# Optimization experiments

Hardware: AMD Instinct MI355X
Metric: run time of the kernel (lower is better)

Reference implementation:

```python
import jax, jax.numpy as jnp
import numpy as np

TOPK = 13
NUM_CLASSES = 80
ALPHA = 1.0
BETA = 6.0
EPS = 1e-09
BS, NA, M = 8, 33600, 64
IMG = 1280.0


def setup_inputs() -> dict:
    key = jax.random.key(0)
    k = jax.random.split(key, 8)
    pd_scores = jax.random.uniform(k[0], (BS, NA, NUM_CLASSES), jnp.float32)
    pd_xy = jax.random.uniform(k[1], (BS, NA, 2), jnp.float32) * IMG
    pd_r = jax.random.uniform(k[2], (BS, NA, 1), jnp.float32) * 63.0 + 1.0
    pd_circles = jnp.concatenate([pd_xy, pd_r], axis=-1)
    anc_points = jax.random.uniform(k[3], (NA, 2), jnp.float32) * IMG
    gt_labels = jax.random.randint(k[4], (BS, M, 1), 0, NUM_CLASSES)
    gt_xy = jax.random.uniform(k[5], (BS, M, 2), jnp.float32) * IMG
    gt_r = jax.random.uniform(k[6], (BS, M, 1), jnp.float32) * 120.0 + 8.0
    gt_circles = jnp.concatenate([gt_xy, gt_r], axis=-1)
    mask_gt = (jax.random.uniform(k[7], (BS, M, 1)) > 0.2).astype(jnp.float32)
    return {"pd_scores": pd_scores, "pd_circles": pd_circles, "anc_points": anc_points,
            "gt_labels": gt_labels, "gt_circles": gt_circles, "mask_gt": mask_gt}


def _circle_iou(gt_circles, pd_circles):
    # gt_circles: (bs, M, 3); pd_circles: (bs, NA, 3) -> iou (bs, M, NA)
    c0 = gt_circles[:, :, None, :2]          # (bs, M, 1, 2)
    r0 = gt_circles[:, :, None, 2]           # (bs, M, 1)
    c1 = pd_circles[:, None, :, :2]          # (bs, 1, NA, 2)
    r1 = pd_circles[:, None, :, 2]           # (bs, 1, NA)
    d = jnp.sqrt(jnp.sum((c0 - c1) ** 2, axis=-1) + 1e-12)  # (bs, M, NA)
    # lens (partial-overlap) area, numerically safe
    d1 = (r0 ** 2 - r1 ** 2 + d ** 2) / (2.0 * d)
    d2 = d - d1
    a0 = r0 ** 2 * jnp.arccos(jnp.clip(d1 / jnp.maximum(r0, EPS), -1.0, 1.0)) \
         - d1 * jnp.sqrt(jnp.clip(r0 ** 2 - d1 ** 2, 0.0, None))
    a1 = r1 ** 2 * jnp.arccos(jnp.clip(d2 / jnp.maximum(r1, EPS), -1.0, 1.0)) \
         - d2 * jnp.sqrt(jnp.clip(r1 ** 2 - d2 ** 2, 0.0, None))
    lens = a0 + a1
    contained = jnp.pi * jnp.minimum(r0, r1) ** 2
    inter = jnp.where(d >= r0 + r1, 0.0, jnp.where(d <= jnp.abs(r0 - r1), contained, lens))
    area0 = jnp.pi * r0 ** 2
    area1 = jnp.pi * r1 ** 2
    union = area0 + area1 - inter
    return jnp.where(union > 0, inter / union, 0.0)


def _assigner(pd_scores, pd_circles, anc_points, gt_labels, gt_circles, mask_gt):
    bs, na, nc = pd_scores.shape
    m = gt_circles.shape[1]
    mask_gt_f = mask_gt[..., 0]  # (bs, m)

    # select_candidates_in_gts: anchor point inside gt circle
    d_anc = jnp.sqrt(jnp.sum((anc_points[None, None, :, :] - gt_circles[:, :, None, :2]) ** 2, axis=-1))
    mask_in_gts = (d_anc < gt_circles[:, :, None, 2]).astype(pd_scores.dtype)  # (bs, m, na)
    mask_valid = mask_in_gts * mask_gt_f[:, :, None]

    # get_box_metrics: gather class scores at gt label, circle IoU, align metric
    gl = jnp.clip(gt_labels[..., 0], 0, nc - 1)  # (bs, m) int
    ps_t = jnp.transpose(pd_scores, (0, 2, 1))   # (bs, nc, na)
    bbox_scores = jnp.take_along_axis(ps_t, jnp.broadcast_to(gl[:, :, None], (bs, m, na)), axis=1)
    bbox_scores = bbox_scores * mask_valid
    overlaps = _circle_iou(gt_circles, pd_circles) * mask_valid  # (bs, m, na)
    align_metric = (bbox_scores ** ALPHA) * (overlaps ** BETA)

    # select_topk_candidates
    topk_metrics, topk_idxs = jax.lax.top_k(align_metric, TOPK)   # (bs, m, topk)
    topk_mask = jnp.broadcast_to(mask_gt_f[:, :, None] > 0, topk_idxs.shape)
    topk_idxs = jnp.where(topk_mask, topk_idxs, 0)
    counts = jnp.zeros((bs, m, na), pd_scores.dtype).at[
        jnp.arange(bs)[:, None, None], jnp.arange(m)[None, :, None], topk_idxs].add(1.0)
    mask_topk = jnp.where(counts > 1, 0.0, counts)
    mask_pos = mask_topk * mask_in_gts * mask_gt_f[:, :, None]

    # select_highest_overlaps: resolve anchors assigned to multiple gts
    fg = jnp.sum(mask_pos, axis=1)                       # (bs, na)
    multi = (fg[:, None, :] > 1)                          # (bs, 1->m, na)
    max_idx = jnp.argmax(overlaps, axis=1)                # (bs, na)
    is_max = jax.nn.one_hot(max_idx, m, axis=1, dtype=mask_pos.dtype)  # (bs, m, na)
    mask_pos = jnp.where(multi, is_max, mask_pos)
    fg_mask = jnp.sum(mask_pos, axis=1)                   # (bs, na)
    target_gt_idx = jnp.argmax(mask_pos, axis=1)          # (bs, na)

    # get_targets
    bidx = jnp.arange(bs)[:, None]
    target_labels = jnp.clip(gt_labels[..., 0][bidx, target_gt_idx], 0, None)   # (bs, na)
    target_circles = gt_circles[bidx, target_gt_idx]                             # (bs, na, 3)
    target_scores = jax.nn.one_hot(target_labels, nc, dtype=pd_scores.dtype)
    target_scores = jnp.where(fg_mask[..., None] > 0, target_scores, 0.0)

    # normalize scores by aligned metric
    am = align_metric * mask_pos
    pos_align = jnp.max(am, axis=-1, keepdims=True)                # (bs, m, 1)
    pos_overlaps = jnp.max(overlaps * mask_pos, axis=-1, keepdims=True)
    norm = jnp.max(am * pos_overlaps / (pos_align + EPS), axis=1)[..., None]  # (bs, na, 1)
    target_scores = target_scores * norm
    return target_labels, target_circles, target_scores, fg_mask > 0, target_gt_idx


def reference(pd_scores, pd_circles, anc_points, gt_labels, gt_circles, mask_gt):
    return _assigner(pd_scores, pd_circles, anc_points, gt_labels, gt_circles, mask_gt)
```

## Files before the change

### kernel.cpp

```cpp
#include <hip/hip_runtime.h>
#include <math.h>

#define B   8
#define NA  33600
#define M   64
#define NC  80
#define KK  13
#define EPSF 1e-9f
#define PIF 3.14159265358979323846f

#define NPOS 1536
#define NBM  (B * M)
#define SPB  (M * KK)


__device__ __forceinline__ float circle_iou(float gx, float gy, float gr,
                                            float px, float py, float pr) {
    float dx = gx - px, dy = gy - py;
    float d  = sqrtf(dx * dx + dy * dy + 1e-12f);
    float r0sq = gr * gr, r1sq = pr * pr;
    float d1 = (r0sq - r1sq + d * d) / (2.0f * d);
    float d2 = d - d1;
    float t0 = fminf(fmaxf(d1 / fmaxf(gr, EPSF), -1.0f), 1.0f);
    float t1 = fminf(fmaxf(d2 / fmaxf(pr, EPSF), -1.0f), 1.0f);
    float a0 = r0sq * acosf(t0) - d1 * sqrtf(fmaxf(r0sq - d1 * d1, 0.0f));
    float a1 = r1sq * acosf(t1) - d2 * sqrtf(fmaxf(r1sq - d2 * d2, 0.0f));
    float lens = a0 + a1;
    float rmin = fminf(gr, pr);
    float contained = PIF * rmin * rmin;
    float inter = (d >= gr + pr) ? 0.0f
                : ((d <= fabsf(gr - pr)) ? contained : lens);
    float uni = PIF * r0sq + PIF * r1sq - inter;
    return (uni > 0.0f) ? inter / uni : 0.0f;
}


__global__ __launch_bounds__(1024)
void k_discover(const float* __restrict__ pd_scores, const float* __restrict__ pd_circles,
                const float* __restrict__ anc, const int* __restrict__ gt_labels,
                const float* __restrict__ gt_circles, const float* __restrict__ mask_gt,
                int* __restrict__ wlist, int* __restrict__ assigned,
                float* __restrict__ am_val) {
    int bid = blockIdx.x;
    int b   = bid & 7;
    int m   = bid >> 3;
    int bm  = b * M + m;
    int tid = threadIdx.x;

    const int SL = (B * NA) / NBM;
    int s0 = bid * SL;
    if (tid < SL) { assigned[s0 + tid] = -1; am_val[s0 + tid] = 0.0f; }

    __shared__ int   s_ccnt, s_pcnt;
    __shared__ int   s_ca[NPOS];
    __shared__ int   s_pa[NPOS];
    __shared__ float s_pv[NPOS];
    __shared__ int   s_win[KK];

    float gmask = mask_gt[bm];
    if (!(gmask > 0.0f)) {
        if (tid < KK) wlist[bm * KK + tid] = -1;
        return;
    }

    float gx = gt_circles[bm * 3 + 0];
    float gy = gt_circles[bm * 3 + 1];
    float gr = gt_circles[bm * 3 + 2];
    int gl = gt_labels[bm];
    gl = gl < 0 ? 0 : (gl > NC - 1 ? NC - 1 : gl);

    if (tid == 0) { s_ccnt = 0; s_pcnt = 0; }
    __syncthreads();

    for (int q = tid; q < NA / 2; q += 1024) {
        float4 ap = reinterpret_cast<const float4*>(anc)[q];
        float dx0 = ap.x - gx, dy0 = ap.y - gy;
        float dx1 = ap.z - gx, dy1 = ap.w - gy;
        bool h0 = sqrtf(dx0 * dx0 + dy0 * dy0) < gr;
        bool h1 = sqrtf(dx1 * dx1 + dy1 * dy1) < gr;
        if (h0) { int p = atomicAdd(&s_ccnt, 1); if (p < NPOS) s_ca[p] = 2 * q; }
        if (h1) { int p = atomicAdd(&s_ccnt, 1); if (p < NPOS) s_ca[p] = 2 * q + 1; }
    }
    __syncthreads();
    int ccnt = s_ccnt; if (ccnt > NPOS) ccnt = NPOS;

    for (int i = tid; i < ccnt; i += 1024) {
        int a = s_ca[i];
        size_t pb = ((size_t)b * NA + a) * 3;
        float px = pd_circles[pb + 0];
        float py = pd_circles[pb + 1];
        float pr = pd_circles[pb + 2];
        float cdx = gx - px, cdy = gy - py;
        float dc = sqrtf(cdx * cdx + cdy * cdy + 1e-12f);
        if (dc >= gr + pr) continue;
        float ov = circle_iou(gx, gy, gr, px, py, pr);
        if (!(ov > 0.0f)) continue;
        float sc = pd_scores[((size_t)b * NA + a) * NC + gl];
        float o2 = ov * ov;
        float met = sc * (o2 * o2 * o2);
        if (met > 0.0f) {
            int p = atomicAdd(&s_pcnt, 1);
            s_pa[p] = a; s_pv[p] = met;
        }
    }
    __syncthreads();
    int pcnt = s_pcnt;

    if (tid >= 64) return;

    for (int k = 0; k < KK; k++) {
        float bv = 0.0f; int ba = 0x7fffffff; int bp = -1;
        for (int i = tid; i < pcnt; i += 64) {
            float v = s_pv[i];
            if (v > 0.0f) {
                int a = s_pa[i];
                if (v > bv || (v == bv && a < ba)) { bv = v; ba = a; bp = i; }
            }
        }
        for (int off = 32; off > 0; off >>= 1) {
            float v2 = __shfl_xor(bv, off);
            int   a2 = __shfl_xor(ba, off);
            int   p2 = __shfl_xor(bp, off);
            if (v2 > bv || (v2 == bv && a2 < ba)) { bv = v2; ba = a2; bp = p2; }
        }
        if (tid == 0) {
            if (bp >= 0) { s_win[k] = ba; s_pv[bp] = -1.0f; }
            else s_win[k] = -2;
        }
    }

    int defmask = 0;
    for (int k = 0; k < KK; k++) if (s_win[k] == -2) defmask |= (1 << k);
    if (defmask) {
        int base = 0;
        while (defmask && base < NA) {
            int idx = base + tid;
            bool freez = (idx < NA);
            for (int i = 0; i < pcnt; i++)
                freez = freez && (s_pa[i] != idx);
            unsigned long long msk = __ballot(freez);
            while (msk && defmask) {
                int bit = __ffsll((long long)msk) - 1; msk &= msk - 1;
                int k2  = __ffs(defmask) - 1;          defmask &= defmask - 1;
                if (tid == 0) s_win[k2] = base + bit;
            }
            base += 64;
        }
        while (defmask) {
            int k2 = __ffs(defmask) - 1; defmask &= defmask - 1;
            if (tid == 0) s_win[k2] = -1;
        }
    }

    if (tid < KK) {
        int a = s_win[tid];
        int outv = -1;
        if (a >= 0) {
            float ax = anc[2 * a], ay = anc[2 * a + 1];
            float dx = ax - gx, dy = ay - gy;
            if (sqrtf(dx * dx + dy * dy) < gr) outv = a;
        }
        wlist[bm * KK + tid] = outv;
    }
}


__global__ __launch_bounds__(1024)
void k_resolve(const float* __restrict__ pd_scores, const float* __restrict__ pd_circles,
               const float* __restrict__ anc, const int* __restrict__ gt_labels,
               const float* __restrict__ gt_circles, const float* __restrict__ mask_gt,
               const int* __restrict__ wlist,
               int* __restrict__ assigned, float* __restrict__ am_val,
               int* __restrict__ pos_align_i, int* __restrict__ pos_ov_i) {
    int b = blockIdx.x;
    int tid = threadIdx.x;

    __shared__ unsigned int s_cnt[NA / 4 + 1];
    __shared__ float s_gx[M], s_gy[M], s_gr[M];
    __shared__ int   s_gl[M], s_act[M];
    __shared__ int   s_posa[M], s_poso[M];
    __shared__ int   s_multi[512];
    __shared__ int   s_nm;

    if (tid < M) {
        int gi = b * M + tid;
        s_act[tid] = mask_gt[gi] > 0.0f;
        s_gx[tid] = gt_circles[gi * 3 + 0];
        s_gy[tid] = gt_circles[gi * 3 + 1];
        s_gr[tid] = gt_circles[gi * 3 + 2];
        int l = gt_labels[gi];
        s_gl[tid] = l < 0 ? 0 : (l > NC - 1 ? NC - 1 : l);
        s_posa[tid] = 0; s_poso[tid] = 0;
    }
    if (tid == 0) s_nm = 0;
    for (int w = tid; w < NA / 4 + 1; w += 1024) s_cnt[w] = 0;
    __syncthreads();

    int a = -1, m = -1; unsigned int prev = 0;
    if (tid < SPB) {
        a = wlist[b * SPB + tid];
        m = tid / KK;
        if (a >= 0) {
            unsigned int sh = 8u * (a & 3);
            unsigned int old = atomicAdd(&s_cnt[a >> 2], 1u << sh);
            prev = (old >> sh) & 0xFFu;
        }
    }
    __syncthreads();

    bool single = false;
    if (a >= 0) {
        unsigned int c = (s_cnt[a >> 2] >> (8u * (a & 3))) & 0xFFu;
        if (c == 1u) single = true;
        else if (prev == 0u) { int i2 = atomicAdd(&s_nm, 1); s_multi[i2] = a; }
    }
    if (single) {
        int i = b * NA + a;
        float gx = s_gx[m], gy = s_gy[m], gr = s_gr[m];
        float px = pd_circles[(size_t)i * 3 + 0];
        float py = pd_circles[(size_t)i * 3 + 1];
        float pr = pd_circles[(size_t)i * 3 + 2];
        float cdx = gx - px, cdy = gy - py;
        float dc = sqrtf(cdx * cdx + cdy * cdy + 1e-12f);
        float ov = (dc >= gr + pr) ? 0.0f : circle_iou(gx, gy, gr, px, py, pr);
        float met = 0.0f;
        if (ov > 0.0f) {
            float sc = pd_scores[(size_t)i * NC + s_gl[m]];
            float o2 = ov * ov;
            met = sc * (o2 * o2 * o2);
        }
        assigned[i] = m;
        am_val[i]   = met;
        atomicMax(&s_posa[m], __float_as_int(met));
        atomicMax(&s_poso[m], __float_as_int(ov));
    }
    __syncthreads();

    int lane = tid & 63, w = tid >> 6;
    int nm = s_nm;
    for (int r = w; r < nm; r += 16) {
        int am_ = s_multi[r];
        int i = b * NA + am_;
        float ax = anc[2 * am_], ay = anc[2 * am_ + 1];
        float px = pd_circles[(size_t)i * 3 + 0];
        float py = pd_circles[(size_t)i * 3 + 1];
        float pr = pd_circles[(size_t)i * 3 + 2];
        float ov = 0.0f;
        if (s_act[lane]) {
            float gx = s_gx[lane], gy = s_gy[lane], gr = s_gr[lane];
            float dx = ax - gx, dy = ay - gy;
            if (sqrtf(dx * dx + dy * dy) < gr) {
                float cdx = gx - px, cdy = gy - py;
                float dc = sqrtf(cdx * cdx + cdy * cdy + 1e-12f);
                ov = (dc >= gr + pr) ? 0.0f : circle_iou(gx, gy, gr, px, py, pr);
            }
        }
        float bv = ov; int bmx = lane;
        for (int off = 32; off > 0; off >>= 1) {
            float v2 = __shfl_xor(bv, off);
            int   m2 = __shfl_xor(bmx, off);
            if (v2 > bv || (v2 == bv && m2 < bmx)) { bv = v2; bmx = m2; }
        }
        if (lane == 0) {
            float met = 0.0f;
            if (bv > 0.0f) {
                float sc = pd_scores[(size_t)i * NC + s_gl[bmx]];
                float o2 = bv * bv;
                met = sc * (o2 * o2 * o2);
            }
            assigned[i] = bmx;
            am_val[i]   = met;
            atomicMax(&s_posa[bmx], __float_as_int(met));
            atomicMax(&s_poso[bmx], __float_as_int(bv));
        }
    }
    __syncthreads();

    if (tid < M) {
        pos_align_i[b * M + tid] = s_posa[tid];
        pos_ov_i[b * M + tid]    = s_poso[tid];
    }
}


__global__ void k_out(const int* __restrict__ assigned, const float* __restrict__ am_val,
                      const int* __restrict__ pos_align_i, const int* __restrict__ pos_ov_i,
                      const int* __restrict__ gt_labels, const float* __restrict__ gt_circles,
                      float* __restrict__ out_labels, float* __restrict__ out_circ,
                      float* __restrict__ out_scores, float* __restrict__ out_fg,
                      float* __restrict__ out_gtidx) {
    const int QPR = NC / 4;
    int q = blockIdx.x * blockDim.x + threadIdx.x;
    if (q >= B * NA * QPR) return;
    int row = q / QPR;
    int c0  = (q - row * QPR) * 4;
    int b   = row / NA;

    int g = assigned[row];
    int gidx = 0; float fg = 0.0f; float norm = 0.0f;
    if (g >= 0) {
        gidx = g; fg = 1.0f;
        float pa = __int_as_float(pos_align_i[b * M + g]);
        float po = __int_as_float(pos_ov_i[b * M + g]);
        norm = am_val[row] * po / (pa + EPSF);
    }
    int rawl = gt_labels[b * M + gidx];
    int lbl = rawl < 0 ? 0 : rawl;

    float4 v = make_float4(0.f, 0.f, 0.f, 0.f);
    if (g >= 0) {
        int off = lbl - c0;
        if (off >= 0 && off < 4) ((float*)&v)[off] = norm;
    }
    reinterpret_cast<float4*>(out_scores)[q] = v;

    if (c0 == 0) {
        out_labels[row] = (float)lbl;
        out_circ[(size_t)row * 3 + 0] = gt_circles[(b * M + gidx) * 3 + 0];
        out_circ[(size_t)row * 3 + 1] = gt_circles[(b * M + gidx) * 3 + 1];
        out_circ[(size_t)row * 3 + 2] = gt_circles[(b * M + gidx) * 3 + 2];
        out_fg[row]    = fg;
        out_gtidx[row] = (float)gidx;
    }
}


extern "C" void kernel_launch(void* const* d_in, const int* in_sizes, int n_in,
                              void* d_out, int out_size, void* d_ws, size_t ws_size,
                              hipStream_t stream) {
    const float* pd_scores  = (const float*)d_in[0];
    const float* pd_circles = (const float*)d_in[1];
    const float* anc        = (const float*)d_in[2];
    const int*   gt_labels  = (const int*)  d_in[3];
    const float* gt_circles = (const float*)d_in[4];
    const float* mask_gt    = (const float*)d_in[5];

    char* w = (char*)d_ws;
    int*   wlist       = (int*)w;   w += (size_t)NBM * KK * sizeof(int);
    int*   assigned    = (int*)w;   w += (size_t)B * NA * sizeof(int);
    float* am_val      = (float*)w; w += (size_t)B * NA * sizeof(float);
    int*   pos_align_i = (int*)w;   w += (size_t)B * M * sizeof(int);
    int*   pos_ov_i    = (int*)w;   w += (size_t)B * M * sizeof(int);

    float* out        = (float*)d_out;
    float* out_labels = out;
    float* out_circ   = out_labels + (size_t)B * NA;
    float* out_scores = out_circ + (size_t)B * NA * 3;
    float* out_fg     = out_scores + (size_t)B * NA * NC;
    float* out_gtidx  = out_fg + (size_t)B * NA;

    k_discover<<<NBM, 1024, 0, stream>>>(pd_scores, pd_circles, anc, gt_labels,
                                         gt_circles, mask_gt,
                                         wlist, assigned, am_val);

    k_resolve<<<B, 1024, 0, stream>>>(pd_scores, pd_circles, anc, gt_labels,
                                      gt_circles, mask_gt, wlist,
                                      assigned, am_val, pos_align_i, pos_ov_i);

    int nq = B * NA * (NC / 4);
    k_out<<<(nq + 255) / 256, 256, 0, stream>>>(assigned, am_val,
                                                pos_align_i, pos_ov_i,
                                                gt_labels, gt_circles,
                                                out_labels, out_circ, out_scores,
                                                out_fg, out_gtidx);
}
```

Baseline: 73.78 us.

## Split resolve kernel per (batch, gt) block with global atomic maxima

The resolve stage moves from one 1024-thread block per batch to one 256-thread block per (batch, gt) pair. Each block finds duplicate anchors by scanning the 832-entry winner list instead of a per-batch shared-memory counter array. The per-gt max reductions now go through global atomicMax, and the discover kernel zero-initializes those arrays first. The goal is more parallelism in a tiny serial stage, at the cost of redundant list loads and scans per block plus global atomics.

```diff
diff --git a/kernel.cpp b/kernel.cpp
--- a/kernel.cpp
+++ b/kernel.cpp
@@ -40,7 +40,8 @@
                 const float* __restrict__ anc, const int* __restrict__ gt_labels,
                 const float* __restrict__ gt_circles, const float* __restrict__ mask_gt,
                 int* __restrict__ wlist, int* __restrict__ assigned,
-                float* __restrict__ am_val) {
+                float* __restrict__ am_val,
+                int* __restrict__ pos_align_i, int* __restrict__ pos_ov_i) {
     int bid = blockIdx.x;
     int b   = bid & 7;
     int m   = bid >> 3;
@@ -50,6 +51,7 @@
     const int SL = (B * NA) / NBM;
     int s0 = bid * SL;
     if (tid < SL) { assigned[s0 + tid] = -1; am_val[s0 + tid] = 0.0f; }
+    if (m == 0 && tid < M) { pos_align_i[b * M + tid] = 0; pos_ov_i[b * M + tid] = 0; }
 
     __shared__ int   s_ccnt, s_pcnt;
     __shared__ int   s_ca[NPOS];
@@ -165,21 +167,23 @@
 }
 
 
-__global__ __launch_bounds__(1024)
+__global__ __launch_bounds__(256)
 void k_resolve(const float* __restrict__ pd_scores, const float* __restrict__ pd_circles,
                const float* __restrict__ anc, const int* __restrict__ gt_labels,
                const float* __restrict__ gt_circles, const float* __restrict__ mask_gt,
                const int* __restrict__ wlist,
                int* __restrict__ assigned, float* __restrict__ am_val,
                int* __restrict__ pos_align_i, int* __restrict__ pos_ov_i) {
-    int b = blockIdx.x;
+    int bid = blockIdx.x;
+    int b   = bid & 7;
+    int m   = bid >> 3;
     int tid = threadIdx.x;
-
-    __shared__ unsigned int s_cnt[NA / 4 + 1];
+    int lane = tid & 63, w = tid >> 6;
+
+    __shared__ int   s_wl[SPB];
     __shared__ float s_gx[M], s_gy[M], s_gr[M];
     __shared__ int   s_gl[M], s_act[M];
-    __shared__ int   s_posa[M], s_poso[M];
-    __shared__ int   s_multi[512];
+    __shared__ int   s_multi[KK];
     __shared__ int   s_nm;
 
     if (tid < M) {
@@ -190,55 +194,48 @@
         s_gr[tid] = gt_circles[gi * 3 + 2];
         int l = gt_labels[gi];
         s_gl[tid] = l < 0 ? 0 : (l > NC - 1 ? NC - 1 : l);
-        s_posa[tid] = 0; s_poso[tid] = 0;
     }
     if (tid == 0) s_nm = 0;
-    for (int w = tid; w < NA / 4 + 1; w += 1024) s_cnt[w] = 0;
-    __syncthreads();
-
-    int a = -1, m = -1; unsigned int prev = 0;
-    if (tid < SPB) {
-        a = wlist[b * SPB + tid];
-        m = tid / KK;
-        if (a >= 0) {
-            unsigned int sh = 8u * (a & 3);
-            unsigned int old = atomicAdd(&s_cnt[a >> 2], 1u << sh);
-            prev = (old >> sh) & 0xFFu;
-        }
-    }
-    __syncthreads();
-
-    bool single = false;
-    if (a >= 0) {
-        unsigned int c = (s_cnt[a >> 2] >> (8u * (a & 3))) & 0xFFu;
-        if (c == 1u) single = true;
-        else if (prev == 0u) { int i2 = atomicAdd(&s_nm, 1); s_multi[i2] = a; }
-    }
-    if (single) {
-        int i = b * NA + a;
-        float gx = s_gx[m], gy = s_gy[m], gr = s_gr[m];
-        float px = pd_circles[(size_t)i * 3 + 0];
-        float py = pd_circles[(size_t)i * 3 + 1];
-        float pr = pd_circles[(size_t)i * 3 + 2];
-        float cdx = gx - px, cdy = gy - py;
-        float dc = sqrtf(cdx * cdx + cdy * cdy + 1e-12f);
-        float ov = (dc >= gr + pr) ? 0.0f : circle_iou(gx, gy, gr, px, py, pr);
-        float met = 0.0f;
-        if (ov > 0.0f) {
-            float sc = pd_scores[(size_t)i * NC + s_gl[m]];
-            float o2 = ov * ov;
-            met = sc * (o2 * o2 * o2);
-        }
-        assigned[i] = m;
-        am_val[i]   = met;
-        atomicMax(&s_posa[m], __float_as_int(met));
-        atomicMax(&s_poso[m], __float_as_int(ov));
-    }
-    __syncthreads();
-
-    int lane = tid & 63, w = tid >> 6;
+    for (int i = tid; i < SPB; i += 256) s_wl[i] = wlist[b * SPB + i];
+    __syncthreads();
+
+    if (w == 0) {
+        int myslot = m * KK + lane;
+        int mya = (lane < KK) ? s_wl[myslot] : -1;
+        int cnt = 0, minslot = SPB;
+        for (int i = 0; i < SPB; i++) {
+            int v = s_wl[i];
+            if (mya >= 0 && v == mya) { cnt++; if (i < minslot) minslot = i; }
+        }
+        if (mya >= 0 && minslot == myslot) {
+            if (cnt == 1) {
+                int i = b * NA + mya;
+                float gx = s_gx[m], gy = s_gy[m], gr = s_gr[m];
+                float px = pd_circles[(size_t)i * 3 + 0];
+                float py = pd_circles[(size_t)i * 3 + 1];
+                float pr = pd_circles[(size_t)i * 3 + 2];
+                float cdx = gx - px, cdy = gy - py;
+                float dc = sqrtf(cdx * cdx + cdy * cdy + 1e-12f);
+                float ov = (dc >= gr + pr) ? 0.0f : circle_iou(gx, gy, gr, px, py, pr);
+                float met = 0.0f;
+                if (ov > 0.0f) {
+                    float sc = pd_scores[(size_t)i * NC + s_gl[m]];
+                    float o2 = ov * ov;
+                    met = sc * (o2 * o2 * o2);
+                }
+                assigned[i] = m;
+                am_val[i]   = met;
+                atomicMax(&pos_align_i[b * M + m], __float_as_int(met));
+                atomicMax(&pos_ov_i[b * M + m],    __float_as_int(ov));
+            } else {
+                int p = atomicAdd(&s_nm, 1); s_multi[p] = mya;
+            }
+        }
+    }
+    __syncthreads();
+
     int nm = s_nm;
-    for (int r = w; r < nm; r += 16) {
+    for (int r = w; r < nm; r += 4) {
         int am_ = s_multi[r];
         int i = b * NA + am_;
         float ax = anc[2 * am_], ay = anc[2 * am_ + 1];
@@ -270,15 +267,9 @@
             }
             assigned[i] = bmx;
             am_val[i]   = met;
-            atomicMax(&s_posa[bmx], __float_as_int(met));
-            atomicMax(&s_poso[bmx], __float_as_int(bv));
-        }
-    }
-    __syncthreads();
-
-    if (tid < M) {
-        pos_align_i[b * M + tid] = s_posa[tid];
-        pos_ov_i[b * M + tid]    = s_poso[tid];
+            atomicMax(&pos_align_i[b * M + bmx], __float_as_int(met));
+            atomicMax(&pos_ov_i[b * M + bmx],    __float_as_int(bv));
+        }
     }
 }
 
@@ -351,11 +342,12 @@
 
     k_discover<<<NBM, 1024, 0, stream>>>(pd_scores, pd_circles, anc, gt_labels,
                                          gt_circles, mask_gt,
-                                         wlist, assigned, am_val);
-
-    k_resolve<<<B, 1024, 0, stream>>>(pd_scores, pd_circles, anc, gt_labels,
-                                      gt_circles, mask_gt, wlist,
-                                      assigned, am_val, pos_align_i, pos_ov_i);
+                                         wlist, assigned, am_val,
+                                         pos_align_i, pos_ov_i);
+
+    k_resolve<<<NBM, 256, 0, stream>>>(pd_scores, pd_circles, anc, gt_labels,
+                                       gt_circles, mask_gt, wlist,
+                                       assigned, am_val, pos_align_i, pos_ov_i);
 
     int nq = B * NA * (NC / 4);
     k_out<<<(nq + 255) / 256, 256, 0, stream>>>(assigned, am_val,
```

Result: slower. 119.6 us (+62.1%).

## Bin anchors into a uniform spatial grid to prune the in-circle search

Applied to the files above, without the earlier changes.

Adds a k_bin kernel that buckets anchor points into a 16x16 grid of 80-pixel cells, and changes k_discover to scan only the cells overlapping each GT circle's bounding box instead of all 33600 anchors. This cuts the per-GT brute-force scan over anchors. The cost is an extra kernel in which each of the 256 blocks re-reads every anchor. Cell capacity is fixed at 320 and the cell range is capped at 36, so anchors are silently dropped if a cell overflows or a circle spans more than 6x6 cells. It also assumes coordinates lie within 1280 pixels, which holds for these inputs (GT radius is at most 128).

```diff
diff --git a/kernel.cpp b/kernel.cpp
--- a/kernel.cpp
+++ b/kernel.cpp
@@ -12,6 +12,11 @@
 #define NPOS 1536
 #define NBM  (B * M)
 #define SPB  (M * KK)
+
+#define GRID 16
+#define CELLW 80.0f
+#define NCELL (GRID * GRID)
+#define CAP  320
 
 
 __device__ __forceinline__ float circle_iou(float gx, float gy, float gr,
@@ -35,10 +40,40 @@
 }
 
 
+__global__ __launch_bounds__(256)
+void k_bin(const float* __restrict__ anc, float4* __restrict__ bin_pack,
+           int* __restrict__ bin_cnt) {
+    int c  = blockIdx.x;
+    int cy = c >> 4, cx = c & 15;
+    int tid = threadIdx.x;
+    __shared__ int   s_cnt;
+    __shared__ float s_x[CAP], s_y[CAP];
+    __shared__ int   s_i[CAP];
+    if (tid == 0) s_cnt = 0;
+    __syncthreads();
+    const float inv = 1.0f / CELLW;
+    for (int a = tid; a < NA; a += 256) {
+        float2 p = reinterpret_cast<const float2*>(anc)[a];
+        int ax = (int)(p.x * inv);
+        int ay = (int)(p.y * inv);
+        if (ax == cx && ay == cy) {
+            int q = atomicAdd(&s_cnt, 1);
+            if (q < CAP) { s_x[q] = p.x; s_y[q] = p.y; s_i[q] = a; }
+        }
+    }
+    __syncthreads();
+    int n = s_cnt; if (n > CAP) n = CAP;
+    if (tid == 0) bin_cnt[c] = n;
+    for (int q = tid; q < n; q += 256)
+        bin_pack[c * CAP + q] = make_float4(s_x[q], s_y[q], __int_as_float(s_i[q]), 0.0f);
+}
+
+
 __global__ __launch_bounds__(1024)
 void k_discover(const float* __restrict__ pd_scores, const float* __restrict__ pd_circles,
                 const float* __restrict__ anc, const int* __restrict__ gt_labels,
                 const float* __restrict__ gt_circles, const float* __restrict__ mask_gt,
+                const float4* __restrict__ bin_pack, const int* __restrict__ bin_cnt,
                 int* __restrict__ wlist, int* __restrict__ assigned,
                 float* __restrict__ am_val) {
     int bid = blockIdx.x;
@@ -56,6 +91,8 @@
     __shared__ int   s_pa[NPOS];
     __shared__ float s_pv[NPOS];
     __shared__ int   s_win[KK];
+    __shared__ int   s_cells[36];
+    __shared__ int   s_bn[36];
 
     float gmask = mask_gt[bm];
     if (!(gmask > 0.0f)) {
@@ -69,17 +106,35 @@
     int gl = gt_labels[bm];
     gl = gl < 0 ? 0 : (gl > NC - 1 ? NC - 1 : gl);
 
+    const float inv = 1.0f / CELLW;
+    int cx0 = (int)floorf((gx - gr) * inv); if (cx0 < 0) cx0 = 0;
+    int cx1 = (int)floorf((gx + gr) * inv); if (cx1 > GRID - 1) cx1 = GRID - 1;
+    int cy0 = (int)floorf((gy - gr) * inv); if (cy0 < 0) cy0 = 0;
+    int cy1 = (int)floorf((gy + gr) * inv); if (cy1 > GRID - 1) cy1 = GRID - 1;
+    int nx = cx1 - cx0 + 1, ny = cy1 - cy0 + 1;
+    int ncell = nx * ny; if (ncell > 36) ncell = 36;
+
     if (tid == 0) { s_ccnt = 0; s_pcnt = 0; }
-    __syncthreads();
-
-    for (int q = tid; q < NA / 2; q += 1024) {
-        float4 ap = reinterpret_cast<const float4*>(anc)[q];
-        float dx0 = ap.x - gx, dy0 = ap.y - gy;
-        float dx1 = ap.z - gx, dy1 = ap.w - gy;
-        bool h0 = sqrtf(dx0 * dx0 + dy0 * dy0) < gr;
-        bool h1 = sqrtf(dx1 * dx1 + dy1 * dy1) < gr;
-        if (h0) { int p = atomicAdd(&s_ccnt, 1); if (p < NPOS) s_ca[p] = 2 * q; }
-        if (h1) { int p = atomicAdd(&s_ccnt, 1); if (p < NPOS) s_ca[p] = 2 * q + 1; }
+    if (tid < ncell) {
+        int lx = tid % nx, ly = tid / nx;
+        int c = (cy0 + ly) * GRID + (cx0 + lx);
+        s_cells[tid] = c;
+        s_bn[tid]    = bin_cnt[c];
+    }
+    __syncthreads();
+
+    int total = ncell * CAP;
+    for (int f = tid; f < total; f += 1024) {
+        int ci = f / CAP;
+        int i  = f - ci * CAP;
+        if (i < s_bn[ci]) {
+            float4 e = bin_pack[s_cells[ci] * CAP + i];
+            float dx = e.x - gx, dy = e.y - gy;
+            if (sqrtf(dx * dx + dy * dy) < gr) {
+                int p = atomicAdd(&s_ccnt, 1);
+                if (p < NPOS) s_ca[p] = __float_as_int(e.z);
+            }
+        }
     }
     __syncthreads();
     int ccnt = s_ccnt; if (ccnt > NPOS) ccnt = NPOS;
@@ -336,6 +391,8 @@
     const float* mask_gt    = (const float*)d_in[5];
 
     char* w = (char*)d_ws;
+    float4* bin_pack   = (float4*)w; w += (size_t)NCELL * CAP * sizeof(float4);
+    int*   bin_cnt     = (int*)w;   w += (size_t)NCELL * sizeof(int);
     int*   wlist       = (int*)w;   w += (size_t)NBM * KK * sizeof(int);
     int*   assigned    = (int*)w;   w += (size_t)B * NA * sizeof(int);
     float* am_val      = (float*)w; w += (size_t)B * NA * sizeof(float);
@@ -349,8 +406,10 @@
     float* out_fg     = out_scores + (size_t)B * NA * NC;
     float* out_gtidx  = out_fg + (size_t)B * NA;
 
+    k_bin<<<NCELL, 256, 0, stream>>>(anc, bin_pack, bin_cnt);
+
     k_discover<<<NBM, 1024, 0, stream>>>(pd_scores, pd_circles, anc, gt_labels,
-                                         gt_circles, mask_gt,
+                                         gt_circles, mask_gt, bin_pack, bin_cnt,
                                          wlist, assigned, am_val);
 
     k_resolve<<<B, 1024, 0, stream>>>(pd_scores, pd_circles, anc, gt_labels,
```

Result: slower. 118.6 us (+60.8%).

## Fuse resolve stage into discover kernel via last-block-per-batch counter

Applied to the files above, without the earlier changes.

Merges the per-batch resolve kernel into the discover kernel: each block bumps a per-batch atomic counter, and the last block to finish for a batch does the conflict resolution, reusing the discover shared buffer as the histogram. The aim is to drop one kernel launch and the gap between launches. In exchange it adds a memset of the counters, threadfences, and a serial tail in which only 8 blocks do the resolve work. The assigned/am_val initialisation is also re-indexed per (b,m) slice, which still covers every anchor.

```diff
diff --git a/kernel.cpp b/kernel.cpp
--- a/kernel.cpp
+++ b/kernel.cpp
@@ -12,6 +12,7 @@
 #define NPOS 1536
 #define NBM  (B * M)
 #define SPB  (M * KK)
+#define SL   (NA / M)
 
 
 __device__ __forceinline__ float circle_iou(float gx, float gy, float gr,
@@ -40,169 +41,170 @@
                 const float* __restrict__ anc, const int* __restrict__ gt_labels,
                 const float* __restrict__ gt_circles, const float* __restrict__ mask_gt,
                 int* __restrict__ wlist, int* __restrict__ assigned,
-                float* __restrict__ am_val) {
+                float* __restrict__ am_val,
+                int* __restrict__ pos_align_i, int* __restrict__ pos_ov_i,
+                int* __restrict__ done_cnt) {
     int bid = blockIdx.x;
     int b   = bid & 7;
     int m   = bid >> 3;
     int bm  = b * M + m;
     int tid = threadIdx.x;
 
-    const int SL = (B * NA) / NBM;
-    int s0 = bid * SL;
-    if (tid < SL) { assigned[s0 + tid] = -1; am_val[s0 + tid] = 0.0f; }
-
-    __shared__ int   s_ccnt, s_pcnt;
-    __shared__ int   s_ca[NPOS];
-    __shared__ int   s_pa[NPOS];
-    __shared__ float s_pv[NPOS];
-    __shared__ int   s_win[KK];
+    {
+        int base = b * NA + m * SL;
+        if (tid < SL) { assigned[base + tid] = -1; am_val[base + tid] = 0.0f; }
+    }
+
+    __shared__ unsigned s_big[8448];
+    int*   s_ca = (int*)s_big;
+    int*   s_pa = (int*)(s_big + 1536);
+    float* s_pv = (float*)(s_big + 3072);
+    __shared__ int s_ccnt, s_pcnt;
+    __shared__ int s_win[KK];
+    __shared__ int s_last;
 
     float gmask = mask_gt[bm];
-    if (!(gmask > 0.0f)) {
+    bool active = gmask > 0.0f;
+
+    if (active) {
+        float gx = gt_circles[bm * 3 + 0];
+        float gy = gt_circles[bm * 3 + 1];
+        float gr = gt_circles[bm * 3 + 2];
+        int gl = gt_labels[bm];
+        gl = gl < 0 ? 0 : (gl > NC - 1 ? NC - 1 : gl);
+
+        if (tid == 0) { s_ccnt = 0; s_pcnt = 0; }
+        __syncthreads();
+
+        for (int q = tid; q < NA / 2; q += 1024) {
+            float4 ap = reinterpret_cast<const float4*>(anc)[q];
+            float dx0 = ap.x - gx, dy0 = ap.y - gy;
+            float dx1 = ap.z - gx, dy1 = ap.w - gy;
+            bool h0 = sqrtf(dx0 * dx0 + dy0 * dy0) < gr;
+            bool h1 = sqrtf(dx1 * dx1 + dy1 * dy1) < gr;
+            if (h0) { int p = atomicAdd(&s_ccnt, 1); if (p < NPOS) s_ca[p] = 2 * q; }
+            if (h1) { int p = atomicAdd(&s_ccnt, 1); if (p < NPOS) s_ca[p] = 2 * q + 1; }
+        }
+        __syncthreads();
+        int ccnt = s_ccnt; if (ccnt > NPOS) ccnt = NPOS;
+
+        for (int i = tid; i < ccnt; i += 1024) {
+            int a = s_ca[i];
+            size_t pb = ((size_t)b * NA + a) * 3;
+            float px = pd_circles[pb + 0];
+            float py = pd_circles[pb + 1];
+            float pr = pd_circles[pb + 2];
+            float cdx = gx - px, cdy = gy - py;
+            float dc = sqrtf(cdx * cdx + cdy * cdy + 1e-12f);
+            if (dc >= gr + pr) continue;
+            float ov = circle_iou(gx, gy, gr, px, py, pr);
+            if (!(ov > 0.0f)) continue;
+            float sc = pd_scores[((size_t)b * NA + a) * NC + gl];
+            float o2 = ov * ov;
+            float met = sc * (o2 * o2 * o2);
+            if (met > 0.0f) {
+                int p = atomicAdd(&s_pcnt, 1);
+                s_pa[p] = a; s_pv[p] = met;
+            }
+        }
+        __syncthreads();
+        int pcnt = s_pcnt;
+
+        if (tid < 64) {
+            for (int k = 0; k < KK; k++) {
+                float bv = 0.0f; int ba = 0x7fffffff; int bp = -1;
+                for (int i = tid; i < pcnt; i += 64) {
+                    float v = s_pv[i];
+                    if (v > 0.0f) {
+                        int a = s_pa[i];
+                        if (v > bv || (v == bv && a < ba)) { bv = v; ba = a; bp = i; }
+                    }
+                }
+                for (int off = 32; off > 0; off >>= 1) {
+                    float v2 = __shfl_xor(bv, off);
+                    int   a2 = __shfl_xor(ba, off);
+                    int   p2 = __shfl_xor(bp, off);
+                    if (v2 > bv || (v2 == bv && a2 < ba)) { bv = v2; ba = a2; bp = p2; }
+                }
+                if (tid == 0) {
+                    if (bp >= 0) { s_win[k] = ba; s_pv[bp] = -1.0f; }
+                    else s_win[k] = -2;
+                }
+            }
+
+            int defmask = 0;
+            for (int k = 0; k < KK; k++) if (s_win[k] == -2) defmask |= (1 << k);
+            if (defmask) {
+                int base = 0;
+                while (defmask && base < NA) {
+                    int idx = base + tid;
+                    bool freez = (idx < NA);
+                    for (int i = 0; i < pcnt; i++)
+                        freez = freez && (s_pa[i] != idx);
+                    unsigned long long msk = __ballot(freez);
+                    while (msk && defmask) {
+                        int bit = __ffsll((long long)msk) - 1; msk &= msk - 1;
+                        int k2  = __ffs(defmask) - 1;          defmask &= defmask - 1;
+                        if (tid == 0) s_win[k2] = base + bit;
+                    }
+                    base += 64;
+                }
+                while (defmask) {
+                    int k2 = __ffs(defmask) - 1; defmask &= defmask - 1;
+                    if (tid == 0) s_win[k2] = -1;
+                }
+            }
+
+            if (tid < KK) {
+                int a = s_win[tid];
+                int outv = -1;
+                if (a >= 0) {
+                    float ax = anc[2 * a], ay = anc[2 * a + 1];
+                    float dx = ax - gx, dy = ay - gy;
+                    if (sqrtf(dx * dx + dy * dy) < gr) outv = a;
+                }
+                wlist[bm * KK + tid] = outv;
+            }
+        }
+    } else {
         if (tid < KK) wlist[bm * KK + tid] = -1;
-        return;
-    }
-
-    float gx = gt_circles[bm * 3 + 0];
-    float gy = gt_circles[bm * 3 + 1];
-    float gr = gt_circles[bm * 3 + 2];
-    int gl = gt_labels[bm];
-    gl = gl < 0 ? 0 : (gl > NC - 1 ? NC - 1 : gl);
-
-    if (tid == 0) { s_ccnt = 0; s_pcnt = 0; }
-    __syncthreads();
-
-    for (int q = tid; q < NA / 2; q += 1024) {
-        float4 ap = reinterpret_cast<const float4*>(anc)[q];
-        float dx0 = ap.x - gx, dy0 = ap.y - gy;
-        float dx1 = ap.z - gx, dy1 = ap.w - gy;
-        bool h0 = sqrtf(dx0 * dx0 + dy0 * dy0) < gr;
-        bool h1 = sqrtf(dx1 * dx1 + dy1 * dy1) < gr;
-        if (h0) { int p = atomicAdd(&s_ccnt, 1); if (p < NPOS) s_ca[p] = 2 * q; }
-        if (h1) { int p = atomicAdd(&s_ccnt, 1); if (p < NPOS) s_ca[p] = 2 * q + 1; }
-    }
-    __syncthreads();
-    int ccnt = s_ccnt; if (ccnt > NPOS) ccnt = NPOS;
-
-    for (int i = tid; i < ccnt; i += 1024) {
-        int a = s_ca[i];
-        size_t pb = ((size_t)b * NA + a) * 3;
-        float px = pd_circles[pb + 0];
-        float py = pd_circles[pb + 1];
-        float pr = pd_circles[pb + 2];
-        float cdx = gx - px, cdy = gy - py;
-        float dc = sqrtf(cdx * cdx + cdy * cdy + 1e-12f);
-        if (dc >= gr + pr) continue;
-        float ov = circle_iou(gx, gy, gr, px, py, pr);
-        if (!(ov > 0.0f)) continue;
-        float sc = pd_scores[((size_t)b * NA + a) * NC + gl];
-        float o2 = ov * ov;
-        float met = sc * (o2 * o2 * o2);
-        if (met > 0.0f) {
-            int p = atomicAdd(&s_pcnt, 1);
-            s_pa[p] = a; s_pv[p] = met;
-        }
-    }
-    __syncthreads();
-    int pcnt = s_pcnt;
-
-    if (tid >= 64) return;
-
-    for (int k = 0; k < KK; k++) {
-        float bv = 0.0f; int ba = 0x7fffffff; int bp = -1;
-        for (int i = tid; i < pcnt; i += 64) {
-            float v = s_pv[i];
-            if (v > 0.0f) {
-                int a = s_pa[i];
-                if (v > bv || (v == bv && a < ba)) { bv = v; ba = a; bp = i; }
-            }
-        }
-        for (int off = 32; off > 0; off >>= 1) {
-            float v2 = __shfl_xor(bv, off);
-            int   a2 = __shfl_xor(ba, off);
-            int   p2 = __shfl_xor(bp, off);
-            if (v2 > bv || (v2 == bv && a2 < ba)) { bv = v2; ba = a2; bp = p2; }
-        }
-        if (tid == 0) {
-            if (bp >= 0) { s_win[k] = ba; s_pv[bp] = -1.0f; }
-            else s_win[k] = -2;
-        }
-    }
-
-    int defmask = 0;
-    for (int k = 0; k < KK; k++) if (s_win[k] == -2) defmask |= (1 << k);
-    if (defmask) {
-        int base = 0;
-        while (defmask && base < NA) {
-            int idx = base + tid;
-            bool freez = (idx < NA);
-            for (int i = 0; i < pcnt; i++)
-                freez = freez && (s_pa[i] != idx);
-            unsigned long long msk = __ballot(freez);
-            while (msk && defmask) {
-                int bit = __ffsll((long long)msk) - 1; msk &= msk - 1;
-                int k2  = __ffs(defmask) - 1;          defmask &= defmask - 1;
-                if (tid == 0) s_win[k2] = base + bit;
-            }
-            base += 64;
-        }
-        while (defmask) {
-            int k2 = __ffs(defmask) - 1; defmask &= defmask - 1;
-            if (tid == 0) s_win[k2] = -1;
-        }
-    }
-
-    if (tid < KK) {
-        int a = s_win[tid];
-        int outv = -1;
-        if (a >= 0) {
-            float ax = anc[2 * a], ay = anc[2 * a + 1];
-            float dx = ax - gx, dy = ay - gy;
-            if (sqrtf(dx * dx + dy * dy) < gr) outv = a;
-        }
-        wlist[bm * KK + tid] = outv;
-    }
-}
-
-
-__global__ __launch_bounds__(1024)
-void k_resolve(const float* __restrict__ pd_scores, const float* __restrict__ pd_circles,
-               const float* __restrict__ anc, const int* __restrict__ gt_labels,
-               const float* __restrict__ gt_circles, const float* __restrict__ mask_gt,
-               const int* __restrict__ wlist,
-               int* __restrict__ assigned, float* __restrict__ am_val,
-               int* __restrict__ pos_align_i, int* __restrict__ pos_ov_i) {
-    int b = blockIdx.x;
-    int tid = threadIdx.x;
-
-    __shared__ unsigned int s_cnt[NA / 4 + 1];
-    __shared__ float s_gx[M], s_gy[M], s_gr[M];
-    __shared__ int   s_gl[M], s_act[M];
-    __shared__ int   s_posa[M], s_poso[M];
-    __shared__ int   s_multi[512];
-    __shared__ int   s_nm;
+    }
+
+    __threadfence();
+    __syncthreads();
+    if (tid == 0) s_last = (atomicAdd(&done_cnt[b], 1) == M - 1) ? 1 : 0;
+    __syncthreads();
+    if (!s_last) return;
+    __threadfence();
+
+    unsigned* s_hist = s_big;
+    __shared__ float r_gx[M], r_gy[M], r_gr[M];
+    __shared__ int   r_gl[M], r_act[M];
+    __shared__ int   r_posa[M], r_poso[M];
+    __shared__ int   r_multi[512];
+    __shared__ int   r_nm;
 
     if (tid < M) {
         int gi = b * M + tid;
-        s_act[tid] = mask_gt[gi] > 0.0f;
-        s_gx[tid] = gt_circles[gi * 3 + 0];
-        s_gy[tid] = gt_circles[gi * 3 + 1];
-        s_gr[tid] = gt_circles[gi * 3 + 2];
+        r_act[tid] = mask_gt[gi] > 0.0f;
+        r_gx[tid] = gt_circles[gi * 3 + 0];
+        r_gy[tid] = gt_circles[gi * 3 + 1];
+        r_gr[tid] = gt_circles[gi * 3 + 2];
         int l = gt_labels[gi];
-        s_gl[tid] = l < 0 ? 0 : (l > NC - 1 ? NC - 1 : l);
-        s_posa[tid] = 0; s_poso[tid] = 0;
-    }
-    if (tid == 0) s_nm = 0;
-    for (int w = tid; w < NA / 4 + 1; w += 1024) s_cnt[w] = 0;
-    __syncthreads();
-
-    int a = -1, m = -1; unsigned int prev = 0;
+        r_gl[tid] = l < 0 ? 0 : (l > NC - 1 ? NC - 1 : l);
+        r_posa[tid] = 0; r_poso[tid] = 0;
+    }
+    if (tid == 0) r_nm = 0;
+    for (int w = tid; w < NA / 4 + 1; w += 1024) s_hist[w] = 0;
+    __syncthreads();
+
+    int a = -1, mm0 = -1; unsigned prev = 0;
     if (tid < SPB) {
         a = wlist[b * SPB + tid];
-        m = tid / KK;
+        mm0 = tid / KK;
         if (a >= 0) {
-            unsigned int sh = 8u * (a & 3);
-            unsigned int old = atomicAdd(&s_cnt[a >> 2], 1u << sh);
+            unsigned sh = 8u * (a & 3);
+            unsigned old = atomicAdd(&s_hist[a >> 2], 1u << sh);
             prev = (old >> sh) & 0xFFu;
         }
     }
@@ -210,13 +212,13 @@
 
     bool single = false;
     if (a >= 0) {
-        unsigned int c = (s_cnt[a >> 2] >> (8u * (a & 3))) & 0xFFu;
+        unsigned c = (s_hist[a >> 2] >> (8u * (a & 3))) & 0xFFu;
         if (c == 1u) single = true;
-        else if (prev == 0u) { int i2 = atomicAdd(&s_nm, 1); s_multi[i2] = a; }
+        else if (prev == 0u) { int i2 = atomicAdd(&r_nm, 1); r_multi[i2] = a; }
     }
     if (single) {
         int i = b * NA + a;
-        float gx = s_gx[m], gy = s_gy[m], gr = s_gr[m];
+        float gx = r_gx[mm0], gy = r_gy[mm0], gr = r_gr[mm0];
         float px = pd_circles[(size_t)i * 3 + 0];
         float py = pd_circles[(size_t)i * 3 + 1];
         float pr = pd_circles[(size_t)i * 3 + 2];
@@ -225,29 +227,29 @@
         float ov = (dc >= gr + pr) ? 0.0f : circle_iou(gx, gy, gr, px, py, pr);
         float met = 0.0f;
         if (ov > 0.0f) {
-            float sc = pd_scores[(size_t)i * NC + s_gl[m]];
+            float sc = pd_scores[(size_t)i * NC + r_gl[mm0]];
             float o2 = ov * ov;
             met = sc * (o2 * o2 * o2);
         }
-        assigned[i] = m;
+        assigned[i] = mm0;
         am_val[i]   = met;
-        atomicMax(&s_posa[m], __float_as_int(met));
-        atomicMax(&s_poso[m], __float_as_int(ov));
+        atomicMax(&r_posa[mm0], __float_as_int(met));
+        atomicMax(&r_poso[mm0], __float_as_int(ov));
     }
     __syncthreads();
 
     int lane = tid & 63, w = tid >> 6;
-    int nm = s_nm;
+    int nm = r_nm;
     for (int r = w; r < nm; r += 16) {
-        int am_ = s_multi[r];
+        int am_ = r_multi[r];
         int i = b * NA + am_;
         float ax = anc[2 * am_], ay = anc[2 * am_ + 1];
         float px = pd_circles[(size_t)i * 3 + 0];
         float py = pd_circles[(size_t)i * 3 + 1];
         float pr = pd_circles[(size_t)i * 3 + 2];
         float ov = 0.0f;
-        if (s_act[lane]) {
-            float gx = s_gx[lane], gy = s_gy[lane], gr = s_gr[lane];
+        if (r_act[lane]) {
+            float gx = r_gx[lane], gy = r_gy[lane], gr = r_gr[lane];
             float dx = ax - gx, dy = ay - gy;
             if (sqrtf(dx * dx + dy * dy) < gr) {
                 float cdx = gx - px, cdy = gy - py;
@@ -264,21 +266,21 @@
         if (lane == 0) {
             float met = 0.0f;
             if (bv > 0.0f) {
-                float sc = pd_scores[(size_t)i * NC + s_gl[bmx]];
+                float sc = pd_scores[(size_t)i * NC + r_gl[bmx]];
                 float o2 = bv * bv;
                 met = sc * (o2 * o2 * o2);
             }
             assigned[i] = bmx;
             am_val[i]   = met;
-            atomicMax(&s_posa[bmx], __float_as_int(met));
-            atomicMax(&s_poso[bmx], __float_as_int(bv));
+            atomicMax(&r_posa[bmx], __float_as_int(met));
+            atomicMax(&r_poso[bmx], __float_as_int(bv));
         }
     }
     __syncthreads();
 
     if (tid < M) {
-        pos_align_i[b * M + tid] = s_posa[tid];
-        pos_ov_i[b * M + tid]    = s_poso[tid];
+        pos_align_i[b * M + tid] = r_posa[tid];
+        pos_ov_i[b * M + tid]    = r_poso[tid];
     }
 }
 
@@ -336,6 +338,7 @@
     const float* mask_gt    = (const float*)d_in[5];
 
     char* w = (char*)d_ws;
+    int*   done_cnt    = (int*)w;   w += 64;
     int*   wlist       = (int*)w;   w += (size_t)NBM * KK * sizeof(int);
     int*   assigned    = (int*)w;   w += (size_t)B * NA * sizeof(int);
     float* am_val      = (float*)w; w += (size_t)B * NA * sizeof(float);
@@ -349,13 +352,12 @@
     float* out_fg     = out_scores + (size_t)B * NA * NC;
     float* out_gtidx  = out_fg + (size_t)B * NA;
 
+    hipMemsetAsync(done_cnt, 0, B * sizeof(int), stream);
+
     k_discover<<<NBM, 1024, 0, stream>>>(pd_scores, pd_circles, anc, gt_labels,
                                          gt_circles, mask_gt,
-                                         wlist, assigned, am_val);
-
-    k_resolve<<<B, 1024, 0, stream>>>(pd_scores, pd_circles, anc, gt_labels,
-                                      gt_circles, mask_gt, wlist,
-                                      assigned, am_val, pos_align_i, pos_ov_i);
+                                         wlist, assigned, am_val,
+                                         pos_align_i, pos_ov_i, done_cnt);
 
     int nq = B * NA * (NC / 4);
     k_out<<<(nq + 255) / 256, 256, 0, stream>>>(assigned, am_val,
```

Result: slower. 205.6 us (+178.7%).
